# Kernel optimization log

Hardware: AMD Instinct MI355X
Metric: run time of the kernel (lower is better)

The kernel has to match this reference:

```python
import jax, jax.numpy as jnp
import numpy as np

NUM_PL, NUM_TR, NUM_AR = 50000, 100000, 10000
HID, FEAT, NUM_LAYERS = 64, 128, 2


def setup_inputs() -> dict:
    key = jax.random.key(0)
    ks = jax.random.split(key, 16)
    inp = {
        'track_x': jax.random.normal(ks[0], (NUM_TR, FEAT), dtype=jnp.float32),
        'pl_tr_src': jax.random.randint(ks[1], (2000000,), 0, NUM_PL, dtype=jnp.int32),
        'pl_tr_dst': jax.random.randint(ks[2], (2000000,), 0, NUM_TR, dtype=jnp.int32),
        'tr_ar_src': jax.random.randint(ks[3], (100000,), 0, NUM_TR, dtype=jnp.int32),
        'tr_ar_dst': jax.random.randint(ks[4], (100000,), 0, NUM_AR, dtype=jnp.int32),
        # learned parameters
        'playlist_emb': jax.random.normal(ks[5], (NUM_PL, HID), dtype=jnp.float32),
        'artist_emb': jax.random.normal(ks[6], (NUM_AR, HID), dtype=jnp.float32),
        'track_W': jax.random.normal(ks[7], (HID, FEAT), dtype=jnp.float32) / np.sqrt(FEAT),
        'track_b': jnp.zeros((HID,), dtype=jnp.float32),
        'type_emb': jax.random.normal(ks[8], (3, HID), dtype=jnp.float32),
        # SAGEConv params per layer: lin_l (neighbor, with bias), lin_r (root, no bias)
        'conv_Wl': jax.random.normal(ks[9], (NUM_LAYERS, HID, HID), dtype=jnp.float32) / np.sqrt(HID),
        'conv_bl': jnp.zeros((NUM_LAYERS, HID), dtype=jnp.float32),
        'conv_Wr': jax.random.normal(ks[10], (NUM_LAYERS, HID, HID), dtype=jnp.float32) / np.sqrt(HID),
    }
    return inp


def reference(track_x, pl_tr_src, pl_tr_dst, tr_ar_src, tr_ar_dst,
              playlist_emb, artist_emb, track_W, track_b, type_emb,
              conv_Wl, conv_bl, conv_Wr):
    off_tr = NUM_PL
    off_ar = NUM_PL + NUM_TR
    N = NUM_PL + NUM_TR + NUM_AR

    # node features: [playlist_emb; track_lin(track_x); artist_emb] + type_emb[type]
    x_tr = track_x @ track_W.T + track_b
    x = jnp.concatenate([playlist_emb, x_tr, artist_emb], axis=0)
    type_ids = jnp.concatenate([
        jnp.zeros((NUM_PL,), jnp.int32),
        jnp.ones((NUM_TR,), jnp.int32),
        jnp.full((NUM_AR,), 2, jnp.int32)])
    x = x + type_emb[type_ids]

    # combined edge index: pl->tr, tr->pl, tr->ar, ar->tr (global node ids)
    pl = pl_tr_src
    tr1 = pl_tr_dst + off_tr
    tr2 = tr_ar_src + off_tr
    ar = tr_ar_dst + off_ar
    src = jnp.concatenate([pl, tr1, tr2, ar])
    dst = jnp.concatenate([tr1, pl, ar, tr2])

    # mean-aggregation degrees (clamped to avoid div by 0)
    deg = jax.ops.segment_sum(jnp.ones_like(src, dtype=x.dtype), dst, num_segments=N)
    deg = jnp.maximum(deg, 1.0)[:, None]

    for l in range(NUM_LAYERS):
        agg = jax.ops.segment_sum(x[src], dst, num_segments=N) / deg  # mean over neighbors
        x = jax.nn.relu(agg @ conv_Wl[l].T + conv_bl[l] + x @ conv_Wr[l].T)

    return (x[:off_tr], x[off_tr:off_ar], x[off_ar:])
```

## Files before the change

### kernel.cpp

```cpp
#include <hip/hip_runtime.h>

#define NUM_PL 50000
#define NUM_TR 100000
#define NUM_AR 10000
#define NN     160000
#define HID    64
#define FEAT   128
#define E_PLTR 2000000
#define E_TRAR 100000
#define E_TOT  4200000
#define OFF_TR 50000
#define OFF_AR 150000

#define BIN_CHUNK 8192
#define NBLK_BIN  513
#define NBUCK     625
#define TABW      626
#define PKD_CAP   (NBLK_BIN * BIN_CHUNK)

#define WSTR 65

__device__ __forceinline__ float h2f(ushort u) {
  _Float16 h = __builtin_bit_cast(_Float16, u);
  return (float)h;
}
__device__ __forceinline__ ushort f2h(float f) {
  _Float16 h = (_Float16)f;
  return __builtin_bit_cast(ushort, h);
}

__device__ __forceinline__ void fmix_lo(float& a, uint u) {
  asm("v_fma_mix_f32 %0, %1, 1.0, %0 op_sel_hi:[1,0,0]"
      : "+v"(a) : "v"(u));
}
__device__ __forceinline__ void fmix_hi(float& a, uint u) {
  asm("v_fma_mix_f32 %0, %1, 1.0, %0 op_sel:[1,0,0] op_sel_hi:[1,0,0]"
      : "+v"(a) : "v"(u));
}
__device__ __forceinline__ void acc_h4(float4& a, ushort4 u) {
  uint2 w = __builtin_bit_cast(uint2, u);
  fmix_lo(a.x, w.x); fmix_hi(a.y, w.x);
  fmix_lo(a.z, w.y); fmix_hi(a.w, w.y);
}

__device__ __forceinline__ void edge_sd(
    int e, const int* __restrict__ pls, const int* __restrict__ pld,
    const int* __restrict__ tas, const int* __restrict__ tad, int& s, int& d) {
  if (e < E_PLTR)                   { s = pls[e];               d = pld[e] + OFF_TR; }
  else if (e < 2 * E_PLTR)          { int i = e - E_PLTR;
                                      s = pld[i] + OFF_TR;      d = pls[i]; }
  else if (e < 2 * E_PLTR + E_TRAR) { int i = e - 2 * E_PLTR;
                                      s = tas[i] + OFF_TR;      d = tad[i] + OFF_AR; }
  else                              { int i = e - 2 * E_PLTR - E_TRAR;
                                      s = tad[i] + OFF_AR;      d = tas[i] + OFF_TR; }
}

__global__ __launch_bounds__(256) void k_init_emb(
    const float* __restrict__ pl_emb, const float* __restrict__ ar_emb,
    const float* __restrict__ type_emb, float* __restrict__ x,
    ushort* __restrict__ xh) {
  int tid = blockIdx.x * 256 + threadIdx.x;
  int f = tid & (HID - 1);
  if (tid < NUM_PL * HID) {
    float v = pl_emb[tid] + type_emb[f];
    x[tid] = v;
    xh[tid] = f2h(v);
  } else {
    int idx = tid - NUM_PL * HID;
    if (idx < NUM_AR * HID) {
      float v = ar_emb[idx] + type_emb[2 * HID + f];
      x[OFF_AR * HID + idx] = v;
      xh[OFF_AR * HID + idx] = f2h(v);
    }
  }
}

__global__ __launch_bounds__(256) void k_track_lin(
    const float* __restrict__ tx, const float* __restrict__ W,
    const float* __restrict__ b, const float* __restrict__ type_emb,
    float* __restrict__ x, ushort* __restrict__ xh) {
  __shared__ float WS[FEAT * 65];
  __shared__ float bs[HID];
  int t = threadIdx.x;
  for (int idx = t; idx < HID * FEAT; idx += 256) {
    int j = idx >> 7, k = idx & (FEAT - 1);
    WS[k * 65 + j] = W[idx];
  }
  if (t < HID) bs[t] = b[t] + type_emb[HID + t];
  __syncthreads();

  int j  = t & 63;
  int wv = __builtin_amdgcn_readfirstlane(t >> 6);
  int row0 = blockIdx.x * 32 + wv * 8;
  const float* xr = tx + (size_t)row0 * FEAT;

  float acc[8] = {0.f, 0.f, 0.f, 0.f, 0.f, 0.f, 0.f, 0.f};
#pragma unroll 4
  for (int k = 0; k < FEAT; ++k) {
    float w = WS[k * 65 + j];
#pragma unroll
    for (int r = 0; r < 8; ++r)
      acc[r] += xr[r * FEAT + k] * w;
  }
#pragma unroll
  for (int r = 0; r < 8; ++r) {
    float v = acc[r] + bs[j];
    x[(OFF_TR + row0 + r) * HID + j] = v;
    xh[(OFF_TR + row0 + r) * HID + j] = f2h(v);
  }
}

__global__ __launch_bounds__(256) void k_bin(
    const int* __restrict__ pls, const int* __restrict__ pld,
    const int* __restrict__ tas, const int* __restrict__ tad,
    int* __restrict__ pkd, int* __restrict__ tab) {
  __shared__ int hist[TABW];
  __shared__ int offs[TABW];
  __shared__ int scanbuf[256];
  int t = threadIdx.x;
  int blk = blockIdx.x;
  int e0 = blk * BIN_CHUNK;
  int e1 = e0 + BIN_CHUNK; if (e1 > E_TOT) e1 = E_TOT;

  for (int i = t; i < TABW; i += 256) hist[i] = 0;
  __syncthreads();

  for (int e = e0 + t; e < e1; e += 256) {
    int s, d; edge_sd(e, pls, pld, tas, tad, s, d);
    int b = min(max(d >> 8, 0), NBUCK - 1);
    atomicAdd(&hist[b], 1);
  }
  __syncthreads();

  int i0 = 3 * t, i1 = 3 * t + 1, i2 = 3 * t + 2;
  int h0 = (i0 < NBUCK) ? hist[i0] : 0;
  int h1 = (i1 < NBUCK) ? hist[i1] : 0;
  int h2 = (i2 < NBUCK) ? hist[i2] : 0;
  int lsum = h0 + h1 + h2;
  scanbuf[t] = lsum;
  __syncthreads();
  int incl = lsum;
#pragma unroll
  for (int off = 1; off < 256; off <<= 1) {
    int add = (t >= off) ? scanbuf[t - off] : 0;
    __syncthreads();
    incl += add;
    scanbuf[t] = incl;
    __syncthreads();
  }
  int base = incl - lsum;
  if (i0 < TABW) offs[i0] = base;
  if (i1 < TABW) offs[i1] = base + h0;
  if (i2 < TABW) offs[i2] = base + h0 + h1;
  __syncthreads();

  for (int i = t; i < TABW; i += 256) tab[blk * TABW + i] = e0 + offs[i];
  for (int i = t; i < NBUCK; i += 256) hist[i] = offs[i];
  __syncthreads();

  for (int e = e0 + t; e < e1; e += 256) {
    int s, d; edge_sd(e, pls, pld, tas, tad, s, d);
    int b = min(max(d >> 8, 0), NBUCK - 1);
    int pos = atomicAdd(&hist[b], 1);
    int idx = min(max(e0 + pos, 0), PKD_CAP - 1);
    pkd[idx] = ((d & 255) << 18) | s;
  }
}

__global__ __launch_bounds__(256) void k_btot(
    const int* __restrict__ tab, int* __restrict__ btot) {
  int b = blockIdx.x * 256 + threadIdx.x;
  if (b >= NBUCK) return;
  int sum = 0;
#pragma unroll 8
  for (int blk = 0; blk < NBLK_BIN; ++blk)
    sum += tab[blk * TABW + b + 1] - tab[blk * TABW + b];
  btot[b] = sum;
}

__global__ __launch_bounds__(1024) void k_bscan(int* __restrict__ btot) {
  __shared__ int s[1024];
  int t = threadIdx.x;
  int val = (t < NBUCK) ? btot[t] : 0;
  s[t] = val;
  __syncthreads();
  int incl = val;
#pragma unroll
  for (int off = 1; off < 1024; off <<= 1) {
    int add = (t >= off) ? s[t - off] : 0;
    __syncthreads();
    incl += add;
    s[t] = incl;
    __syncthreads();
  }
  if (t < NBUCK) btot[t] = incl - val;
}

__global__ __launch_bounds__(256) void k_fill3(
    const int* __restrict__ tab, const int* __restrict__ pkd,
    const int* __restrict__ btot, int* __restrict__ rowptr,
    int* __restrict__ col) {
  __shared__ int cnt[256];
  __shared__ int scanbuf[256];
  int t = threadIdx.x;
  int b = blockIdx.x;
  cnt[t] = 0;
  __syncthreads();

  for (int blk = t; blk < NBLK_BIN; blk += 256) {
    int s0 = tab[blk * TABW + b];
    int s1 = tab[blk * TABW + b + 1];
    s0 = min(max(s0, 0), PKD_CAP);
    s1 = min(max(s1, s0), PKD_CAP);
    for (int i = s0; i < s1; ++i) {
      int doff = (pkd[i] >> 18) & 255;
      atomicAdd(&cnt[doff], 1);
    }
  }
  __syncthreads();

  int val = cnt[t];
  scanbuf[t] = val;
  __syncthreads();
  int incl = val;
#pragma unroll
  for (int off = 1; off < 256; off <<= 1) {
    int add = (t >= off) ? scanbuf[t - off] : 0;
    __syncthreads();
    incl += add;
    scanbuf[t] = incl;
    __syncthreads();
  }
  int rp = btot[b] + incl - val;
  rowptr[(b << 8) + t] = rp;
  if (b == NBUCK - 1 && t == 255) rowptr[NN] = E_TOT;
  __syncthreads();
  cnt[t] = rp;
  __syncthreads();

  for (int blk = t; blk < NBLK_BIN; blk += 256) {
    int s0 = tab[blk * TABW + b];
    int s1 = tab[blk * TABW + b + 1];
    s0 = min(max(s0, 0), PKD_CAP);
    s1 = min(max(s1, s0), PKD_CAP);
    for (int i = s0; i < s1; ++i) {
      int pk = pkd[i];
      int doff = (pk >> 18) & 255;
      int pos = atomicAdd(&cnt[doff], 1);
      pos = min(max(pos, 0), E_TOT - 1);
      col[pos] = pk & 0x3FFFF;
    }
  }
}

__global__ __launch_bounds__(1024, 8) void k_gather_update(
    const int* __restrict__ rowptr, const int* __restrict__ col,
    const ushort* __restrict__ xh,
    const float* __restrict__ Wl, const float* __restrict__ bl,
    const float* __restrict__ Wr,
    ushort* __restrict__ xnh, float* __restrict__ xnf) {
  __shared__ float WlS[HID * WSTR];
  __shared__ float WrS[HID * WSTR];
  __shared__ float bs[HID];
  __shared__ __align__(16) float rowS[16][4][2 * HID];
  int t = threadIdx.x;
  for (int idx = t; idx < HID * HID; idx += 1024) {
    int j = idx >> 6, k = idx & 63;
    WlS[k * WSTR + j] = Wl[idx];
    WrS[k * WSTR + j] = Wr[idx];
  }
  if (t < HID) bs[t] = bl[t];
  __syncthreads();

  int lane = t & 63;
  int wv = t >> 6;
  int r = lane >> 4;
  int c = lane & 15;
  const ushort4* xh4 = (const ushort4*)xh;
  int nbase = (blockIdx.x * 16 + wv) * 4;

  for (int it = 0; it < 4; ++it) {
    int n = nbase + it;
    int rp0 = rowptr[n], rp1 = rowptr[n + 1];

    ushort4 ru;
    if (r == 0) ru = xh4[n * 16 + c];

    float4 a0 = {0.f, 0.f, 0.f, 0.f};
    float4 a1 = {0.f, 0.f, 0.f, 0.f};
    float4 a2 = {0.f, 0.f, 0.f, 0.f};
    float4 a3 = {0.f, 0.f, 0.f, 0.f};
    int base = rp0;
    for (; base + 16 <= rp1; base += 16) {
      int s0 = col[base + r];
      int s1 = col[base + 4 + r];
      int s2 = col[base + 8 + r];
      int s3 = col[base + 12 + r];
      ushort4 u0 = xh4[s0 * 16 + c];
      ushort4 u1 = xh4[s1 * 16 + c];
      ushort4 u2 = xh4[s2 * 16 + c];
      ushort4 u3 = xh4[s3 * 16 + c];
      acc_h4(a0, u0);
      acc_h4(a1, u1);
      acc_h4(a2, u2);
      acc_h4(a3, u3);
    }
    if (base + 4 <= rp1) {
      int s0 = col[base + r];
      acc_h4(a0, xh4[s0 * 16 + c]);
      base += 4;
    }
    if (base + 4 <= rp1) {
      int s1 = col[base + r];
      acc_h4(a1, xh4[s1 * 16 + c]);
      base += 4;
    }
    if (base + 4 <= rp1) {
      int s2 = col[base + r];
      acc_h4(a2, xh4[s2 * 16 + c]);
      base += 4;
    }
    if (base + r < rp1) {
      int s3 = col[base + r];
      acc_h4(a3, xh4[s3 * 16 + c]);
    }
    float4 a;
    a.x = (a0.x + a1.x) + (a2.x + a3.x);
    a.y = (a0.y + a1.y) + (a2.y + a3.y);
    a.z = (a0.z + a1.z) + (a2.z + a3.z);
    a.w = (a0.w + a1.w) + (a2.w + a3.w);
    a.x += __shfl_xor(a.x, 16); a.y += __shfl_xor(a.y, 16);
    a.z += __shfl_xor(a.z, 16); a.w += __shfl_xor(a.w, 16);
    a.x += __shfl_xor(a.x, 32); a.y += __shfl_xor(a.y, 32);
    a.z += __shfl_xor(a.z, 32); a.w += __shfl_xor(a.w, 32);

    if (r == 0) {
      float id = 1.0f / (float)max(rp1 - rp0, 1);
      float4 o;
      o.x = a.x * id; o.y = a.y * id; o.z = a.z * id; o.w = a.w * id;
      float4 rootf;
      rootf.x = h2f(ru.x); rootf.y = h2f(ru.y);
      rootf.z = h2f(ru.z); rootf.w = h2f(ru.w);
      ((float4*)&rowS[wv][it][0])[c] = o;
      ((float4*)&rowS[wv][it][0])[16 + c] = rootf;
    }
  }

  asm volatile("s_waitcnt lgkmcnt(0)" ::: "memory");
  __builtin_amdgcn_sched_barrier(0);

  const float4* row0 = (const float4*)&rowS[wv][0][0];
  const float4* row1 = (const float4*)&rowS[wv][1][0];
  const float4* row2 = (const float4*)&rowS[wv][2][0];
  const float4* row3 = (const float4*)&rowS[wv][3][0];
  float acc0 = 0.f, acc1 = 0.f, acc2 = 0.f, acc3 = 0.f;
#pragma unroll 2
  for (int k4 = 0; k4 < 16; ++k4) {
    float4 g0 = row0[k4], t0 = row0[16 + k4];
    float4 g1 = row1[k4], t1 = row1[16 + k4];
    float4 g2 = row2[k4], t2 = row2[16 + k4];
    float4 g3 = row3[k4], t3 = row3[16 + k4];
    int k = k4 * 4;
    float wl0 = WlS[(k + 0) * WSTR + lane], wr0 = WrS[(k + 0) * WSTR + lane];
    float wl1 = WlS[(k + 1) * WSTR + lane], wr1 = WrS[(k + 1) * WSTR + lane];
    float wl2 = WlS[(k + 2) * WSTR + lane], wr2 = WrS[(k + 2) * WSTR + lane];
    float wl3 = WlS[(k + 3) * WSTR + lane], wr3 = WrS[(k + 3) * WSTR + lane];
    acc0 += g0.x * wl0 + g0.y * wl1 + g0.z * wl2 + g0.w * wl3
          + t0.x * wr0 + t0.y * wr1 + t0.z * wr2 + t0.w * wr3;
    acc1 += g1.x * wl0 + g1.y * wl1 + g1.z * wl2 + g1.w * wl3
          + t1.x * wr0 + t1.y * wr1 + t1.z * wr2 + t1.w * wr3;
    acc2 += g2.x * wl0 + g2.y * wl1 + g2.z * wl2 + g2.w * wl3
          + t2.x * wr0 + t2.y * wr1 + t2.z * wr2 + t2.w * wr3;
    acc3 += g3.x * wl0 + g3.y * wl1 + g3.z * wl2 + g3.w * wl3
          + t3.x * wr0 + t3.y * wr1 + t3.z * wr2 + t3.w * wr3;
  }
  float bias = bs[lane];
  float o0 = fmaxf(acc0 + bias, 0.f);
  float o1 = fmaxf(acc1 + bias, 0.f);
  float o2 = fmaxf(acc2 + bias, 0.f);
  float o3 = fmaxf(acc3 + bias, 0.f);
  if (xnf) {
    xnf[(nbase + 0) * HID + lane] = o0;
    xnf[(nbase + 1) * HID + lane] = o1;
    xnf[(nbase + 2) * HID + lane] = o2;
    xnf[(nbase + 3) * HID + lane] = o3;
  } else {
    xnh[(nbase + 0) * HID + lane] = f2h(o0);
    xnh[(nbase + 1) * HID + lane] = f2h(o1);
    xnh[(nbase + 2) * HID + lane] = f2h(o2);
    xnh[(nbase + 3) * HID + lane] = f2h(o3);
  }
}

extern "C" void kernel_launch(void* const* d_in, const int* in_sizes, int n_in,
                              void* d_out, int out_size, void* d_ws, size_t ws_size,
                              hipStream_t stream) {
  const float* track_x  = (const float*)d_in[0];
  const int*   pl_tr_s  = (const int*)d_in[1];
  const int*   pl_tr_d  = (const int*)d_in[2];
  const int*   tr_ar_s  = (const int*)d_in[3];
  const int*   tr_ar_d  = (const int*)d_in[4];
  const float* pl_emb   = (const float*)d_in[5];
  const float* ar_emb   = (const float*)d_in[6];
  const float* track_W  = (const float*)d_in[7];
  const float* track_b  = (const float*)d_in[8];
  const float* type_emb = (const float*)d_in[9];
  const float* conv_Wl  = (const float*)d_in[10];
  const float* conv_bl  = (const float*)d_in[11];
  const float* conv_Wr  = (const float*)d_in[12];

  float* x = (float*)d_out;

  char* w = (char*)d_ws;
  ushort* xh1   = (ushort*)w;
  int*   pkd    = (int*)w;
  int*   tab    = (int*)(w + (size_t)PKD_CAP * 4);
  w += (size_t)NN * HID * 2;
  ushort* xh0   = (ushort*)w; w += (size_t)NN * HID * 2;
  int*   col    = (int*)w;    w += (size_t)E_TOT * 4;
  int*   rowptr = (int*)w;    w += (size_t)(NN + 1) * 4;
  int*   btot   = (int*)w;

  k_init_emb<<<(NUM_PL + NUM_AR) * HID / 256, 256, 0, stream>>>(
      pl_emb, ar_emb, type_emb, x, xh0);
  k_track_lin<<<NUM_TR / 32, 256, 0, stream>>>(
      track_x, track_W, track_b, type_emb, x, xh0);

  k_bin<<<NBLK_BIN, 256, 0, stream>>>(
      pl_tr_s, pl_tr_d, tr_ar_s, tr_ar_d, pkd, tab);
  k_btot<<<(NBUCK + 255) / 256, 256, 0, stream>>>(tab, btot);
  k_bscan<<<1, 1024, 0, stream>>>(btot);
  k_fill3<<<NBUCK, 256, 0, stream>>>(tab, pkd, btot, rowptr, col);

  k_gather_update<<<NN / 64, 1024, 0, stream>>>(
      rowptr, col, xh0, conv_Wl, conv_bl, conv_Wr, xh1, nullptr);
  k_gather_update<<<NN / 64, 1024, 0, stream>>>(
      rowptr, col, xh1, conv_Wl + HID * HID, conv_bl + HID,
      conv_Wr + HID * HID, xh0 , x);
}
```

Measured before the change: 670.9 us.

## Stage bucket edges in LDS during CSR fill and fold bucket totals into binning

The bucket-total kernel is removed: each binning block now atomically adds its per-bucket histogram into a zeroed global array, which saves one launch and a strided pass over the table. The fill kernel now prefix-scans each thread's segment lengths and copies the packed edges into a shared-memory staging buffer during the counting pass. The scatter pass then reads from LDS instead of re-reading scattered global segments, with a fallback to global reads for segments that overflow the buffer. The roughly 46 KB staging buffer lowers occupancy of the fill kernel, and the global atomics add contention in binning.

```diff
diff --git a/kernel.cpp b/kernel.cpp
--- a/kernel.cpp
+++ b/kernel.cpp
@@ -19,6 +19,8 @@
 #define PKD_CAP   (NBLK_BIN * BIN_CHUNK)
 
 #define WSTR 65
+
+#define SCAP 11520
 
 __device__ __forceinline__ float h2f(ushort u) {
   _Float16 h = __builtin_bit_cast(_Float16, u);
@@ -113,7 +115,7 @@
 __global__ __launch_bounds__(256) void k_bin(
     const int* __restrict__ pls, const int* __restrict__ pld,
     const int* __restrict__ tas, const int* __restrict__ tad,
-    int* __restrict__ pkd, int* __restrict__ tab) {
+    int* __restrict__ pkd, int* __restrict__ tab, int* __restrict__ btot) {
   __shared__ int hist[TABW];
   __shared__ int offs[TABW];
   __shared__ int scanbuf[256];
@@ -136,6 +138,9 @@
   int h0 = (i0 < NBUCK) ? hist[i0] : 0;
   int h1 = (i1 < NBUCK) ? hist[i1] : 0;
   int h2 = (i2 < NBUCK) ? hist[i2] : 0;
+  if (i0 < NBUCK && h0) atomicAdd(&btot[i0], h0);
+  if (i1 < NBUCK && h1) atomicAdd(&btot[i1], h1);
+  if (i2 < NBUCK && h2) atomicAdd(&btot[i2], h2);
   int lsum = h0 + h1 + h2;
   scanbuf[t] = lsum;
   __syncthreads();
@@ -167,17 +172,6 @@
   }
 }
 
-__global__ __launch_bounds__(256) void k_btot(
-    const int* __restrict__ tab, int* __restrict__ btot) {
-  int b = blockIdx.x * 256 + threadIdx.x;
-  if (b >= NBUCK) return;
-  int sum = 0;
-#pragma unroll 8
-  for (int blk = 0; blk < NBLK_BIN; ++blk)
-    sum += tab[blk * TABW + b + 1] - tab[blk * TABW + b];
-  btot[b] = sum;
-}
-
 __global__ __launch_bounds__(1024) void k_bscan(int* __restrict__ btot) {
   __shared__ int s[1024];
   int t = threadIdx.x;
@@ -200,32 +194,69 @@
     const int* __restrict__ tab, const int* __restrict__ pkd,
     const int* __restrict__ btot, int* __restrict__ rowptr,
     int* __restrict__ col) {
+  __shared__ int stage[SCAP];
   __shared__ int cnt[256];
   __shared__ int scanbuf[256];
+  __shared__ int validS;
   int t = threadIdx.x;
   int b = blockIdx.x;
+
+  int s0a = tab[t * TABW + b],         s1a = tab[t * TABW + b + 1];
+  int s0b = tab[(t + 256) * TABW + b], s1b = tab[(t + 256) * TABW + b + 1];
+  int s0c = 0, s1c = 0;
+  if (t + 512 < NBLK_BIN) {
+    s0c = tab[(t + 512) * TABW + b];   s1c = tab[(t + 512) * TABW + b + 1];
+  }
+  s0a = min(max(s0a, 0), PKD_CAP); s1a = min(max(s1a, s0a), PKD_CAP);
+  s0b = min(max(s0b, 0), PKD_CAP); s1b = min(max(s1b, s0b), PKD_CAP);
+  s0c = min(max(s0c, 0), PKD_CAP); s1c = min(max(s1c, s0c), PKD_CAP);
+  int len = (s1a - s0a) + (s1b - s0b) + (s1c - s0c);
+
   cnt[t] = 0;
-  __syncthreads();
-
-  for (int blk = t; blk < NBLK_BIN; blk += 256) {
-    int s0 = tab[blk * TABW + b];
-    int s1 = tab[blk * TABW + b + 1];
-    s0 = min(max(s0, 0), PKD_CAP);
-    s1 = min(max(s1, s0), PKD_CAP);
-    for (int i = s0; i < s1; ++i) {
-      int doff = (pkd[i] >> 18) & 255;
-      atomicAdd(&cnt[doff], 1);
-    }
+  if (t == 0) validS = 0x7fffffff;
+  scanbuf[t] = len;
+  __syncthreads();
+  int incl = len;
+#pragma unroll
+  for (int off = 1; off < 256; off <<= 1) {
+    int add = (t >= off) ? scanbuf[t - off] : 0;
+    __syncthreads();
+    incl += add;
+    scanbuf[t] = incl;
+    __syncthreads();
+  }
+  int base = incl - len;
+  int totalE = scanbuf[255];
+  bool fits = (base + len <= SCAP);
+  if (!fits) atomicMin(&validS, base);
+  __syncthreads();
+  int valid = min(validS, totalE);
+
+  int off = base;
+  for (int i = s0a; i < s1a; ++i) {
+    int pk = pkd[i];
+    atomicAdd(&cnt[(pk >> 18) & 255], 1);
+    if (fits) stage[off++] = pk;
+  }
+  for (int i = s0b; i < s1b; ++i) {
+    int pk = pkd[i];
+    atomicAdd(&cnt[(pk >> 18) & 255], 1);
+    if (fits) stage[off++] = pk;
+  }
+  for (int i = s0c; i < s1c; ++i) {
+    int pk = pkd[i];
+    atomicAdd(&cnt[(pk >> 18) & 255], 1);
+    if (fits) stage[off++] = pk;
   }
   __syncthreads();
 
   int val = cnt[t];
   scanbuf[t] = val;
   __syncthreads();
-  int incl = val;
-#pragma unroll
-  for (int off = 1; off < 256; off <<= 1) {
-    int add = (t >= off) ? scanbuf[t - off] : 0;
+  incl = val;
+#pragma unroll
+  for (int off2 = 1; off2 < 256; off2 <<= 1) {
+    int add = (t >= off2) ? scanbuf[t - off2] : 0;
     __syncthreads();
     incl += add;
     scanbuf[t] = incl;
@@ -238,15 +269,28 @@
   cnt[t] = rp;
   __syncthreads();
 
-  for (int blk = t; blk < NBLK_BIN; blk += 256) {
-    int s0 = tab[blk * TABW + b];
-    int s1 = tab[blk * TABW + b + 1];
-    s0 = min(max(s0, 0), PKD_CAP);
-    s1 = min(max(s1, s0), PKD_CAP);
-    for (int i = s0; i < s1; ++i) {
+  for (int i = t; i < valid; i += 256) {
+    int pk = stage[i];
+    int pos = atomicAdd(&cnt[(pk >> 18) & 255], 1);
+    pos = min(max(pos, 0), E_TOT - 1);
+    col[pos] = pk & 0x3FFFF;
+  }
+  if (!fits) {
+    for (int i = s0a; i < s1a; ++i) {
       int pk = pkd[i];
-      int doff = (pk >> 18) & 255;
-      int pos = atomicAdd(&cnt[doff], 1);
+      int pos = atomicAdd(&cnt[(pk >> 18) & 255], 1);
+      pos = min(max(pos, 0), E_TOT - 1);
+      col[pos] = pk & 0x3FFFF;
+    }
+    for (int i = s0b; i < s1b; ++i) {
+      int pk = pkd[i];
+      int pos = atomicAdd(&cnt[(pk >> 18) & 255], 1);
+      pos = min(max(pos, 0), E_TOT - 1);
+      col[pos] = pk & 0x3FFFF;
+    }
+    for (int i = s0c; i < s1c; ++i) {
+      int pk = pkd[i];
+      int pos = atomicAdd(&cnt[(pk >> 18) & 255], 1);
       pos = min(max(pos, 0), E_TOT - 1);
       col[pos] = pk & 0x3FFFF;
     }
@@ -421,14 +465,15 @@
   int*   rowptr = (int*)w;    w += (size_t)(NN + 1) * 4;
   int*   btot   = (int*)w;
 
+  hipMemsetAsync(btot, 0, NBUCK * sizeof(int), stream);
+
   k_init_emb<<<(NUM_PL + NUM_AR) * HID / 256, 256, 0, stream>>>(
       pl_emb, ar_emb, type_emb, x, xh0);
   k_track_lin<<<NUM_TR / 32, 256, 0, stream>>>(
       track_x, track_W, track_b, type_emb, x, xh0);
 
   k_bin<<<NBLK_BIN, 256, 0, stream>>>(
-      pl_tr_s, pl_tr_d, tr_ar_s, tr_ar_d, pkd, tab);
-  k_btot<<<(NBUCK + 255) / 256, 256, 0, stream>>>(tab, btot);
+      pl_tr_s, pl_tr_d, tr_ar_s, tr_ar_d, pkd, tab, btot);
   k_bscan<<<1, 1024, 0, stream>>>(btot);
   k_fill3<<<NBUCK, 256, 0, stream>>>(tab, pkd, btot, rowptr, col);
 
```

Result: faster. 620.5 us (-7.5%).
